# Performance work log

Measured on AMD Instinct MI355X. Metric: run time of the kernel, lower is better.

Reference implementation:

```python
import jax, jax.numpy as jnp
import numpy as np

N_NODES = 100000
HIDDEN = 64
N_REL = 9
N_LAYERS = 3
N_EDGES = 1000000


def setup_inputs() -> dict:
    key = jax.random.key(0)
    k1, k2, k3, k4, k5 = jax.random.split(key, 5)
    edge_index = jax.random.randint(k1, (2, N_EDGES), 0, N_NODES, dtype=jnp.int64)
    edge_type = jax.random.randint(k2, (N_EDGES,), 0, N_REL, dtype=jnp.int64)
    embeddings = jax.random.uniform(k3, (N_NODES, HIDDEN), dtype=jnp.float32)
    weights = jax.random.uniform(k4, (N_LAYERS, 2 * N_REL, HIDDEN, HIDDEN), dtype=jnp.float32)
    biases = jax.random.uniform(k5, (N_LAYERS, 2 * N_REL, HIDDEN), dtype=jnp.float32)
    return {"edge_index": edge_index, "edge_type": edge_type,
            "embeddings": embeddings, "weights": weights, "biases": biases}


def reference(edge_index, edge_type, embeddings, weights, biases):
    # Faithful translation of RGCNEncoder.forward.
    # NOTE (faithful to source): get_messages always reads self.embeddings,
    # and both `sources` and `dests` are edge_index[d][edge_type == r].
    N, E = embeddings.shape
    L = weights.shape[0]
    R = weights.shape[1] // 2
    idx0 = edge_index[0]          # indices for direction d=0 (source == dest)
    idx1 = edge_index[1]          # indices for direction d=1
    rel0 = edge_type              # weight row r + R*0
    rel1 = edge_type + R          # weight row r + R*1

    output = embeddings
    for l in range(L):
        # Transform every node under every (relation, direction) weight once,
        # then gather per edge. Equivalent to per-relation gather->matmul, but
        # avoids materializing per-edge [E,E] weight matrices.
        T = jnp.einsum('ne,reo->rno', embeddings, weights[l])   # [2R, N, E]
        m0 = T[rel0, idx0] + biases[l][rel0]                    # [n_edges, E]
        m1 = T[rel1, idx1] + biases[l][rel1]                    # [n_edges, E]
        m = jnp.concatenate([m0, m1], axis=0)
        d = jnp.concatenate([idx0, idx1], axis=0)
        # scatter_mean over destination nodes (0 for nodes with no messages)
        s = jax.ops.segment_sum(m, d, num_segments=N)
        cnt = jax.ops.segment_sum(jnp.ones((d.shape[0],), m.dtype), d, num_segments=N)
        hidden = jnp.where(cnt[:, None] > 0, s / jnp.maximum(cnt, 1.0)[:, None], 0.0)
        if l + 1 < L:
            hidden = jax.nn.relu(hidden)
        output = hidden
    return output
```

## Files before the change

### kernel.cpp

```cpp
#include <hip/hip_runtime.h>


typedef float  floatx4 __attribute__((ext_vector_type(4)));
typedef short  shortx8 __attribute__((ext_vector_type(8)));

#define MFMA_BF16(A, B, C) __builtin_amdgcn_mfma_f32_16x16x32_bf16((A), (B), (C), 0, 0, 0)

#define SCAT_GRID 512
#define BKT_CAP   6144

static __device__ __forceinline__ ushort f32_to_bf16_rne(float f) {
    union { float f; unsigned u; } v; v.f = f;
    unsigned r = v.u + 0x7fffu + ((v.u >> 16) & 1u);
    return (ushort)(r >> 16);
}

__global__ void rgcn_prep(const float* __restrict__ w2,
                          const float* __restrict__ b2,
                          ushort* __restrict__ wt_sw,
                          ushort* __restrict__ bias_sw) {
    int i = blockIdx.x * 256 + threadIdx.x;
    const int WELEMS = 18 * 8 * 64 * 8;
    if (i < WELEMS) {
        int r    = i >> 12;
        int rem  = i & 4095;
        int cid  = rem >> 9;
        int lane = (rem >> 3) & 63;
        int j    = i & 7;
        int nt = cid >> 1, kh = cid & 1;
        int o = nt * 16 + (lane & 15);
        int k = kh * 32 + (lane >> 4) * 8 + j;
        wt_sw[i] = f32_to_bf16_rne(w2[(r << 12) + (k << 6) + o]);
    } else {
        int i2 = i - WELEMS;
        if (i2 < 2048) {
            int nt   = i2 >> 9;
            int lane = (i2 >> 3) & 63;
            int j    = i2 & 7;
            int o  = nt * 16 + (lane & 15);
            int rr = (lane >> 4) * 8 + j;
            bias_sw[i2] = (rr < 18) ? f32_to_bf16_rne(b2[rr * 64 + o]) : (ushort)0;
        }
    }
}

__global__ void rgcn_count(const int* __restrict__ ei, const int* __restrict__ et,
                           int* __restrict__ cnts, int E, int N) {
    int e = blockIdx.x * 256 + threadIdx.x;
    if (e < E) {
        int r = et[e];
        int i0 = ei[e];
        int i1 = ei[E + e];
        if ((unsigned)r < 9u) {
            if ((unsigned)i0 < (unsigned)N) atomicAdd(&cnts[i0 * 18 + r], 1);
            if ((unsigned)i1 < (unsigned)N) atomicAdd(&cnts[i1 * 18 + 9 + r], 1);
        }
    }
}

__global__ __launch_bounds__(256) void rgcn_scatter(
    const int* __restrict__ ei,
    const int* __restrict__ et,
    unsigned*  __restrict__ cursors,
    ushort*    __restrict__ bkt,
    int E, int N)
{
    __shared__ unsigned hist[512];
    const int t = threadIdx.x;
    #pragma unroll
    for (int b = t; b < 512; b += 256) hist[b] = 0;
    __syncthreads();

    const int epb = (E + SCAT_GRID - 1) / SCAT_GRID;
    const int e0 = blockIdx.x * epb;
    const int e1 = (e0 + epb < E) ? e0 + epb : E;
    const unsigned KMAX = (unsigned)N * 18u;

    for (int e = e0 + t; e < e1; e += 256) {
        int r = et[e]; int i0 = ei[e]; int i1 = ei[E + e];
        if ((unsigned)r < 9u) {
            unsigned k0 = (unsigned)i0 * 18u + (unsigned)r;
            unsigned k1 = (unsigned)i1 * 18u + 9u + (unsigned)r;
            if (k0 < KMAX) atomicAdd(&hist[k0 >> 12], 1u);
            if (k1 < KMAX) atomicAdd(&hist[k1 >> 12], 1u);
        }
    }
    __syncthreads();

    for (int b = t; b < 512; b += 256) {
        unsigned c = hist[b];
        hist[b] = c ? atomicAdd(&cursors[b], c) : 0u;
    }
    __syncthreads();

    for (int e = e0 + t; e < e1; e += 256) {
        int r = et[e]; int i0 = ei[e]; int i1 = ei[E + e];
        if ((unsigned)r < 9u) {
            unsigned k0 = (unsigned)i0 * 18u + (unsigned)r;
            unsigned k1 = (unsigned)i1 * 18u + 9u + (unsigned)r;
            if (k0 < KMAX) {
                unsigned o = atomicAdd(&hist[k0 >> 12], 1u);
                if (o < BKT_CAP) bkt[(size_t)(k0 >> 12) * BKT_CAP + o] = (ushort)(k0 & 4095u);
            }
            if (k1 < KMAX) {
                unsigned o = atomicAdd(&hist[k1 >> 12], 1u);
                if (o < BKT_CAP) bkt[(size_t)(k1 >> 12) * BKT_CAP + o] = (ushort)(k1 & 4095u);
            }
        }
    }
}

__global__ __launch_bounds__(256) void rgcn_bucket_count(
    const ushort*   __restrict__ bkt,
    const unsigned* __restrict__ cursors,
    int*            __restrict__ cnts,
    int N)
{
    __shared__ int cnt[4096];
    const int t = threadIdx.x;
    const int b = blockIdx.x;
    #pragma unroll
    for (int i = t; i < 4096; i += 256) cnt[i] = 0;
    __syncthreads();

    unsigned n = cursors[b];
    if (n > BKT_CAP) n = BKT_CAP;
    const ushort* bp = bkt + (size_t)b * BKT_CAP;
    for (unsigned i = t; i < n; i += 256)
        atomicAdd(&cnt[bp[i]], 1);
    __syncthreads();

    const int base = b << 12;
    const int lim = N * 18;
    #pragma unroll
    for (int i = t; i < 4096; i += 256)
        if (base + i < lim) cnts[base + i] = cnt[i];
}

__global__ __launch_bounds__(256, 3) void rgcn_main(
    const float*  __restrict__ emb,
    const int*    __restrict__ cnts,
    const ushort* __restrict__ wt_sw,
    const ushort* __restrict__ bias_sw,
    float*        __restrict__ out,
    int N)
{
    __shared__ float  wft[18][128];
    __shared__ ushort wb[128][32];
    __shared__ int    craw[128 * 18];

    const int t    = threadIdx.x;
    const int nb   = blockIdx.x * 128;
    const int wave = t >> 6;
    const int lane = t & 63;
    const int m    = lane & 15;
    const int q    = lane >> 4;

    {
        int lim = (N - nb) * 18;
        if (lim > 2304) lim = 2304;
        #pragma unroll
        for (int j = t; j < 2304; j += 256)
            craw[j] = (j < lim) ? cnts[(size_t)nb * 18 + j] : 0;
    }

    shortx8 af[2][2];
    #pragma unroll
    for (int mt = 0; mt < 2; mt++) {
        int n = nb + wave * 32 + mt * 16 + m;
        if (n >= N) n = N - 1;
        const float* rp = emb + (size_t)n * 64 + q * 8;
        #pragma unroll
        for (int kh = 0; kh < 2; kh++) {
            floatx4 lo = *(const floatx4*)(rp + kh * 32);
            floatx4 hi = *(const floatx4*)(rp + kh * 32 + 4);
            shortx8 f;
            #pragma unroll
            for (int j = 0; j < 4; j++) {
                f[j]     = (short)f32_to_bf16_rne(lo[j]);
                f[j + 4] = (short)f32_to_bf16_rne(hi[j]);
            }
            af[mt][kh] = f;
        }
    }

    const ushort* wbase = wt_sw + (size_t)lane * 8;
    shortx8 bfA[8], bfB[8];
    #pragma unroll
    for (int c = 0; c < 8; c++) bfA[c] = *(const shortx8*)(wbase + c * 512);

    __syncthreads();

    if (t < 128) {
        int c[18];
        int cnt = 0;
        #pragma unroll
        for (int r = 0; r < 18; r++) { c[r] = craw[t * 18 + r]; cnt += c[r]; }
        float inv = (cnt > 0) ? (1.0f / (float)cnt) : 0.0f;
        #pragma unroll
        for (int r = 0; r < 18; r++) {
            float w = (float)c[r] * inv;
            wft[r][t] = w;
            wb[t][r] = f32_to_bf16_rne(w);
        }
        #pragma unroll
        for (int r = 18; r < 32; r++) wb[t][r] = 0;
    }

    __syncthreads();

    floatx4 acc[2][4];
    #pragma unroll
    for (int mt = 0; mt < 2; mt++)
        #pragma unroll
        for (int nt = 0; nt < 4; nt++)
            acc[mt][nt] = (floatx4){0.f, 0.f, 0.f, 0.f};

    for (int r = 0; r < 18; r += 2) {
        {
            const ushort* p = wbase + (r + 1) * 4096;
            #pragma unroll
            for (int c = 0; c < 8; c++) bfB[c] = *(const shortx8*)(p + c * 512);
        }
        {
            floatx4 swv[2];
            #pragma unroll
            for (int mt = 0; mt < 2; mt++)
                swv[mt] = *(const floatx4*)&wft[r][wave * 32 + mt * 16 + q * 4];
            #pragma unroll
            for (int nt = 0; nt < 4; nt++)
                #pragma unroll
                for (int mt = 0; mt < 2; mt++) {
                    floatx4 tmp = (floatx4){0.f, 0.f, 0.f, 0.f};
                    tmp = MFMA_BF16(af[mt][0], bfA[nt * 2 + 0], tmp);
                    tmp = MFMA_BF16(af[mt][1], bfA[nt * 2 + 1], tmp);
                    acc[mt][nt] += swv[mt] * tmp;
                }
        }
        if (r + 2 < 18) {
            const ushort* p = wbase + (r + 2) * 4096;
            #pragma unroll
            for (int c = 0; c < 8; c++) bfA[c] = *(const shortx8*)(p + c * 512);
        }
        {
            floatx4 swv[2];
            #pragma unroll
            for (int mt = 0; mt < 2; mt++)
                swv[mt] = *(const floatx4*)&wft[r + 1][wave * 32 + mt * 16 + q * 4];
            #pragma unroll
            for (int nt = 0; nt < 4; nt++)
                #pragma unroll
                for (int mt = 0; mt < 2; mt++) {
                    floatx4 tmp = (floatx4){0.f, 0.f, 0.f, 0.f};
                    tmp = MFMA_BF16(af[mt][0], bfB[nt * 2 + 0], tmp);
                    tmp = MFMA_BF16(af[mt][1], bfB[nt * 2 + 1], tmp);
                    acc[mt][nt] += swv[mt] * tmp;
                }
        }
    }

    {
        shortx8 wfrag[2];
        #pragma unroll
        for (int mt = 0; mt < 2; mt++)
            wfrag[mt] = *(const shortx8*)&wb[wave * 32 + mt * 16 + m][q * 8];
        #pragma unroll
        for (int nt = 0; nt < 4; nt++) {
            shortx8 btf = *(const shortx8*)(bias_sw + ((size_t)nt * 64 + lane) * 8);
            #pragma unroll
            for (int mt = 0; mt < 2; mt++)
                acc[mt][nt] = MFMA_BF16(wfrag[mt], btf, acc[mt][nt]);
        }
    }

    #pragma unroll
    for (int mt = 0; mt < 2; mt++)
        #pragma unroll
        for (int i = 0; i < 4; i++) {
            int nn = nb + wave * 32 + mt * 16 + q * 4 + i;
            if (nn < N) {
                #pragma unroll
                for (int nt = 0; nt < 4; nt++)
                    out[(size_t)nn * 64 + nt * 16 + m] = acc[mt][nt][i];
            }
        }
}

extern "C" void kernel_launch(void* const* d_in, const int* in_sizes, int n_in,
                              void* d_out, int out_size, void* d_ws, size_t ws_size,
                              hipStream_t stream) {
    const int*   edge_index = (const int*)d_in[0];
    const int*   edge_type  = (const int*)d_in[1];
    const float* emb        = (const float*)d_in[2];
    const float* weights    = (const float*)d_in[3];
    const float* biases     = (const float*)d_in[4];
    float* out = (float*)d_out;

    const int E = in_sizes[1];
    const int N = in_sizes[2] / 64;

    const float* w2 = weights + 2 * 18 * 64 * 64;
    const float* b2 = biases  + 2 * 18 * 64;

    size_t off = 0;
    unsigned* cursors = (unsigned*)((char*)d_ws + off);  off += 512 * 4;
    off = (off + 63) & ~size_t(63);
    int* cnts = (int*)((char*)d_ws + off);               off += (size_t)N * 18 * 4;
    off = (off + 63) & ~size_t(63);
    ushort* bkt = (ushort*)((char*)d_ws + off);          off += (size_t)512 * BKT_CAP * 2;
    off = (off + 63) & ~size_t(63);
    ushort* wt_sw = (ushort*)((char*)d_ws + off);        off += 73728 * 2;
    off = (off + 63) & ~size_t(63);
    ushort* bias_sw = (ushort*)((char*)d_ws + off);      off += 2048 * 2;
    size_t need = off;

    int nbuckets = (N * 18 + 4095) >> 12;

    {
        int total = 18 * 8 * 64 * 8 + 2048;
        rgcn_prep<<<(total + 255) / 256, 256, 0, stream>>>(w2, b2, wt_sw, bias_sw);
    }

    if (ws_size >= need && nbuckets <= 512) {
        hipMemsetAsync(cursors, 0, 512 * 4, stream);
        rgcn_scatter<<<SCAT_GRID, 256, 0, stream>>>(edge_index, edge_type, cursors, bkt, E, N);
        rgcn_bucket_count<<<nbuckets, 256, 0, stream>>>(bkt, cursors, cnts, N);
    } else {
        cnts = (int*)((char*)d_ws + 64);
        wt_sw = (ushort*)((char*)cnts + (size_t)N * 18 * 4);
        bias_sw = wt_sw + 73728;
        rgcn_prep<<<(18 * 8 * 64 * 8 + 2048 + 255) / 256, 256, 0, stream>>>(w2, b2, wt_sw, bias_sw);
        hipMemsetAsync(cnts, 0, (size_t)N * 18 * 4, stream);
        rgcn_count<<<(E + 255) / 256, 256, 0, stream>>>(edge_index, edge_type, cnts, E, N);
    }

    rgcn_main<<<(N + 127) / 128, 256, 0, stream>>>(emb, cnts, wt_sw, bias_sw, out, N);
}
```

Measured before the change: 150.9 us.

## Use per-block LDS bins for edge bucketing and stage weights in LDS

Edge bucketing changes: each scatter block bins its keys into fixed 32-slot LDS bins and writes them out contiguously. This removes the global cursor atomics, the memset and the two-pass histogram, but keys beyond a bin's capacity are silently dropped. Computing the per-node mean weights moves into a separate kernel that writes float and bf16 weight tables to global memory. The main kernel becomes persistent with 512 threads and loads the full bf16 weight set (about 147 KB) into LDS once per block, so weight reads per tile come from LDS rather than global memory. A global-memory fallback remains in case the LDS attribute cannot be set.

```diff
diff --git a/kernel.cpp b/kernel.cpp
--- a/kernel.cpp
+++ b/kernel.cpp
@@ -3,16 +3,24 @@
 
 typedef float  floatx4 __attribute__((ext_vector_type(4)));
 typedef short  shortx8 __attribute__((ext_vector_type(8)));
+typedef unsigned int uint;
 
 #define MFMA_BF16(A, B, C) __builtin_amdgcn_mfma_f32_16x16x32_bf16((A), (B), (C), 0, 0, 0)
 
-#define SCAT_GRID 512
-#define BKT_CAP   6144
+#define NBUF 512
+#define NBKT 512
+#define CAP  32
 
 static __device__ __forceinline__ ushort f32_to_bf16_rne(float f) {
     union { float f; unsigned u; } v; v.f = f;
     unsigned r = v.u + 0x7fffu + ((v.u >> 16) & 1u);
     return (ushort)(r >> 16);
+}
+
+static __device__ __forceinline__ void gload_lds16(const ushort* g, ushort* l) {
+    __builtin_amdgcn_global_load_lds(
+        (const __attribute__((address_space(1))) void*)g,
+        (__attribute__((address_space(3))) void*)l, 16, 0, 0);
 }
 
 __global__ void rgcn_prep(const float* __restrict__ w2,
@@ -44,6 +52,92 @@
     }
 }
 
+__global__ __launch_bounds__(256) void rgcn_scatter(
+    const int* __restrict__ ei,
+    const int* __restrict__ et,
+    ushort*    __restrict__ cursors_g,
+    ushort*    __restrict__ bkt,
+    int E, int N)
+{
+    __shared__ uint   cur[NBKT];
+    __shared__ ushort bins[NBKT][CAP];
+    const int t = threadIdx.x;
+    #pragma unroll
+    for (int b = t; b < NBKT; b += 256) cur[b] = 0;
+    __syncthreads();
+
+    const int epb = (E + NBUF - 1) / NBUF;
+    const int e0 = blockIdx.x * epb;
+    const int e1 = (e0 + epb < E) ? e0 + epb : E;
+    const unsigned KMAX = (unsigned)N * 18u;
+
+    for (int e = e0 + t; e < e1; e += 256) {
+        int r = et[e]; int i0 = ei[e]; int i1 = ei[E + e];
+        if ((unsigned)r < 9u) {
+            unsigned k0 = (unsigned)i0 * 18u + (unsigned)r;
+            unsigned k1 = (unsigned)i1 * 18u + 9u + (unsigned)r;
+            if (k0 < KMAX) {
+                unsigned o = atomicAdd(&cur[k0 >> 12], 1u);
+                if (o < CAP) bins[k0 >> 12][o] = (ushort)(k0 & 4095u);
+            }
+            if (k1 < KMAX) {
+                unsigned o = atomicAdd(&cur[k1 >> 12], 1u);
+                if (o < CAP) bins[k1 >> 12][o] = (ushort)(k1 & 4095u);
+            }
+        }
+    }
+    __syncthreads();
+
+    const uint* b32 = (const uint*)bins;
+    uint* dst = (uint*)bkt;
+    const int blk = blockIdx.x;
+    #pragma unroll
+    for (int idx = t; idx < NBKT * CAP / 2; idx += 256) {
+        int b = idx >> 4;
+        int w = idx & 15;
+        dst[((size_t)b * NBUF + blk) * (CAP / 2) + w] = b32[idx];
+    }
+    #pragma unroll
+    for (int b = t; b < NBKT; b += 256) {
+        uint c = cur[b];
+        cursors_g[(size_t)blk * NBKT + b] = (ushort)(c < CAP ? c : CAP);
+    }
+}
+
+__global__ __launch_bounds__(256) void rgcn_bucket_count(
+    const ushort* __restrict__ bkt,
+    const ushort* __restrict__ cursors_g,
+    int*          __restrict__ cnts,
+    int KMAX)
+{
+    __shared__ int    cnt[4096];
+    __shared__ ushort ccur[NBUF];
+    const int t = threadIdx.x;
+    const int b = blockIdx.x;
+    #pragma unroll
+    for (int i = t; i < 4096; i += 256) cnt[i] = 0;
+    #pragma unroll
+    for (int sb = t; sb < NBUF; sb += 256) ccur[sb] = cursors_g[(size_t)sb * NBKT + b];
+    __syncthreads();
+
+    const uint* src = (const uint*)(bkt + (size_t)b * NBUF * CAP);
+    #pragma unroll
+    for (int idx = t; idx < NBUF * CAP / 2; idx += 256) {
+        int sb = idx >> 4;
+        int w  = idx & 15;
+        unsigned c = ccur[sb];
+        unsigned v = src[idx];
+        if ((unsigned)(2 * w)     < c) atomicAdd(&cnt[v & 4095u], 1);
+        if ((unsigned)(2 * w + 1) < c) atomicAdd(&cnt[(v >> 16) & 4095u], 1);
+    }
+    __syncthreads();
+
+    const int base = b << 12;
+    #pragma unroll
+    for (int i = t; i < 4096; i += 256)
+        if (base + i < KMAX) cnts[base + i] = cnt[i];
+}
+
 __global__ void rgcn_count(const int* __restrict__ ei, const int* __restrict__ et,
                            int* __restrict__ cnts, int E, int N) {
     int e = blockIdx.x * 256 + threadIdx.x;
@@ -58,97 +152,182 @@
     }
 }
 
-__global__ __launch_bounds__(256) void rgcn_scatter(
-    const int* __restrict__ ei,
-    const int* __restrict__ et,
-    unsigned*  __restrict__ cursors,
-    ushort*    __restrict__ bkt,
-    int E, int N)
-{
-    __shared__ unsigned hist[512];
-    const int t = threadIdx.x;
-    #pragma unroll
-    for (int b = t; b < 512; b += 256) hist[b] = 0;
-    __syncthreads();
-
-    const int epb = (E + SCAT_GRID - 1) / SCAT_GRID;
-    const int e0 = blockIdx.x * epb;
-    const int e1 = (e0 + epb < E) ? e0 + epb : E;
-    const unsigned KMAX = (unsigned)N * 18u;
-
-    for (int e = e0 + t; e < e1; e += 256) {
-        int r = et[e]; int i0 = ei[e]; int i1 = ei[E + e];
-        if ((unsigned)r < 9u) {
-            unsigned k0 = (unsigned)i0 * 18u + (unsigned)r;
-            unsigned k1 = (unsigned)i1 * 18u + 9u + (unsigned)r;
-            if (k0 < KMAX) atomicAdd(&hist[k0 >> 12], 1u);
-            if (k1 < KMAX) atomicAdd(&hist[k1 >> 12], 1u);
-        }
-    }
-    __syncthreads();
-
-    for (int b = t; b < 512; b += 256) {
-        unsigned c = hist[b];
-        hist[b] = c ? atomicAdd(&cursors[b], c) : 0u;
-    }
-    __syncthreads();
-
-    for (int e = e0 + t; e < e1; e += 256) {
-        int r = et[e]; int i0 = ei[e]; int i1 = ei[E + e];
-        if ((unsigned)r < 9u) {
-            unsigned k0 = (unsigned)i0 * 18u + (unsigned)r;
-            unsigned k1 = (unsigned)i1 * 18u + 9u + (unsigned)r;
-            if (k0 < KMAX) {
-                unsigned o = atomicAdd(&hist[k0 >> 12], 1u);
-                if (o < BKT_CAP) bkt[(size_t)(k0 >> 12) * BKT_CAP + o] = (ushort)(k0 & 4095u);
-            }
-            if (k1 < KMAX) {
-                unsigned o = atomicAdd(&hist[k1 >> 12], 1u);
-                if (o < BKT_CAP) bkt[(size_t)(k1 >> 12) * BKT_CAP + o] = (ushort)(k1 & 4095u);
-            }
-        }
-    }
-}
-
-__global__ __launch_bounds__(256) void rgcn_bucket_count(
-    const ushort*   __restrict__ bkt,
-    const unsigned* __restrict__ cursors,
-    int*            __restrict__ cnts,
-    int N)
-{
-    __shared__ int cnt[4096];
-    const int t = threadIdx.x;
-    const int b = blockIdx.x;
-    #pragma unroll
-    for (int i = t; i < 4096; i += 256) cnt[i] = 0;
-    __syncthreads();
-
-    unsigned n = cursors[b];
-    if (n > BKT_CAP) n = BKT_CAP;
-    const ushort* bp = bkt + (size_t)b * BKT_CAP;
-    for (unsigned i = t; i < n; i += 256)
-        atomicAdd(&cnt[bp[i]], 1);
-    __syncthreads();
-
-    const int base = b << 12;
-    const int lim = N * 18;
-    #pragma unroll
-    for (int i = t; i < 4096; i += 256)
-        if (base + i < lim) cnts[base + i] = cnt[i];
-}
-
-__global__ __launch_bounds__(256, 3) void rgcn_main(
+__global__ void rgcn_weights(const int* __restrict__ cnts,
+                             float*  __restrict__ wf,
+                             ushort* __restrict__ wb,
+                             int N, int Npad)
+{
+    int n = blockIdx.x * 256 + threadIdx.x;
+    if (n >= Npad) return;
+    float w[18];
+    if (n < N) {
+        int c[18]; int cnt = 0;
+        const int* cp = cnts + (size_t)n * 18;
+        #pragma unroll
+        for (int r = 0; r < 18; r++) { c[r] = cp[r]; cnt += c[r]; }
+        float inv = (cnt > 0) ? (1.0f / (float)cnt) : 0.0f;
+        #pragma unroll
+        for (int r = 0; r < 18; r++) w[r] = (float)c[r] * inv;
+    } else {
+        #pragma unroll
+        for (int r = 0; r < 18; r++) w[r] = 0.0f;
+    }
+    #pragma unroll
+    for (int r = 0; r < 18; r++) wf[(size_t)r * Npad + n] = w[r];
+    ushort pk[32];
+    #pragma unroll
+    for (int r = 0; r < 18; r++) pk[r] = f32_to_bf16_rne(w[r]);
+    #pragma unroll
+    for (int r = 18; r < 32; r++) pk[r] = 0;
+    uint4* dst = (uint4*)(wb + (size_t)n * 32);
+    const uint4* srcp = (const uint4*)pk;
+    #pragma unroll
+    for (int i = 0; i < 4; i++) dst[i] = srcp[i];
+}
+
+static __device__ __forceinline__ void mfma_r_step(
+    const shortx8 af[2][2], const shortx8 bf[8], const floatx4 swv[2], floatx4 acc[2][4])
+{
+    #pragma unroll
+    for (int nt = 0; nt < 4; nt++)
+        #pragma unroll
+        for (int mt = 0; mt < 2; mt++) {
+            floatx4 tmp = (floatx4){0.f, 0.f, 0.f, 0.f};
+            tmp = MFMA_BF16(af[mt][0], bf[nt * 2 + 0], tmp);
+            tmp = MFMA_BF16(af[mt][1], bf[nt * 2 + 1], tmp);
+            acc[mt][nt] += swv[mt] * tmp;
+        }
+}
+
+static __device__ __forceinline__ void load_af(
+    const float* __restrict__ emb, int n, int q, shortx8 af[2])
+{
+    const float* rp = emb + (size_t)n * 64 + q * 8;
+    #pragma unroll
+    for (int kh = 0; kh < 2; kh++) {
+        floatx4 lo = *(const floatx4*)(rp + kh * 32);
+        floatx4 hi = *(const floatx4*)(rp + kh * 32 + 4);
+        shortx8 f;
+        #pragma unroll
+        for (int j = 0; j < 4; j++) {
+            f[j]     = (short)f32_to_bf16_rne(lo[j]);
+            f[j + 4] = (short)f32_to_bf16_rne(hi[j]);
+        }
+        af[kh] = f;
+    }
+}
+
+__global__ __launch_bounds__(512) void rgcn_main_lds(
     const float*  __restrict__ emb,
-    const int*    __restrict__ cnts,
+    const float*  __restrict__ wf,
+    const ushort* __restrict__ wb,
     const ushort* __restrict__ wt_sw,
     const ushort* __restrict__ bias_sw,
     float*        __restrict__ out,
-    int N)
-{
-    __shared__ float  wft[18][128];
-    __shared__ ushort wb[128][32];
-    __shared__ int    craw[128 * 18];
-
+    int N, int Npad, int ntiles)
+{
+    extern __shared__ ushort wlds[];
+
+    const int t    = threadIdx.x;
+    const int wave = t >> 6;
+    const int lane = t & 63;
+    const int m    = lane & 15;
+    const int q    = lane >> 4;
+
+    for (int c = t; c < 9216; c += 512)
+        gload_lds16(wt_sw + (size_t)c * 8, wlds + (size_t)c * 8);
+    __syncthreads();
+
+    const ushort* lbase = wlds + (size_t)lane * 8;
+
+    for (int tile = blockIdx.x; tile < ntiles; tile += gridDim.x) {
+        const int nb = tile * 256;
+
+        shortx8 af[2][2];
+        #pragma unroll
+        for (int mt = 0; mt < 2; mt++) {
+            int n = nb + wave * 32 + mt * 16 + m;
+            if (n >= N) n = N - 1;
+            load_af(emb, n, q, af[mt]);
+        }
+
+        floatx4 acc[2][4];
+        #pragma unroll
+        for (int mt = 0; mt < 2; mt++)
+            #pragma unroll
+            for (int nt = 0; nt < 4; nt++)
+                acc[mt][nt] = (floatx4){0.f, 0.f, 0.f, 0.f};
+
+        const int rowbase = nb + wave * 32;
+
+        shortx8 bA[8], bB[8];
+        #pragma unroll
+        for (int c = 0; c < 8; c++) bA[c] = *(const shortx8*)(lbase + c * 512);
+
+        for (int r = 0; r < 18; r += 2) {
+            {
+                const ushort* p = lbase + (size_t)(r + 1) * 4096;
+                #pragma unroll
+                for (int c = 0; c < 8; c++) bB[c] = *(const shortx8*)(p + c * 512);
+            }
+            {
+                floatx4 swv[2];
+                #pragma unroll
+                for (int mt = 0; mt < 2; mt++)
+                    swv[mt] = *(const floatx4*)(wf + (size_t)r * Npad + rowbase + mt * 16 + q * 4);
+                mfma_r_step(af, bA, swv, acc);
+            }
+            if (r + 2 < 18) {
+                const ushort* p = lbase + (size_t)(r + 2) * 4096;
+                #pragma unroll
+                for (int c = 0; c < 8; c++) bA[c] = *(const shortx8*)(p + c * 512);
+            }
+            {
+                floatx4 swv[2];
+                #pragma unroll
+                for (int mt = 0; mt < 2; mt++)
+                    swv[mt] = *(const floatx4*)(wf + (size_t)(r + 1) * Npad + rowbase + mt * 16 + q * 4);
+                mfma_r_step(af, bB, swv, acc);
+            }
+        }
+
+        {
+            shortx8 wfrag[2];
+            #pragma unroll
+            for (int mt = 0; mt < 2; mt++)
+                wfrag[mt] = *(const shortx8*)(wb + (size_t)(rowbase + mt * 16 + m) * 32 + q * 8);
+            #pragma unroll
+            for (int nt = 0; nt < 4; nt++) {
+                shortx8 btf = *(const shortx8*)(bias_sw + ((size_t)nt * 64 + lane) * 8);
+                #pragma unroll
+                for (int mt = 0; mt < 2; mt++)
+                    acc[mt][nt] = MFMA_BF16(wfrag[mt], btf, acc[mt][nt]);
+            }
+        }
+
+        #pragma unroll
+        for (int mt = 0; mt < 2; mt++)
+            #pragma unroll
+            for (int i = 0; i < 4; i++) {
+                int nn = rowbase + mt * 16 + q * 4 + i;
+                if (nn < N) {
+                    #pragma unroll
+                    for (int nt = 0; nt < 4; nt++)
+                        out[(size_t)nn * 64 + nt * 16 + m] = acc[mt][nt][i];
+                }
+            }
+    }
+}
+
+__global__ __launch_bounds__(256, 3) void rgcn_main_glb(
+    const float*  __restrict__ emb,
+    const float*  __restrict__ wf,
+    const ushort* __restrict__ wb,
+    const ushort* __restrict__ wt_sw,
+    const ushort* __restrict__ bias_sw,
+    float*        __restrict__ out,
+    int N, int Npad)
+{
     const int t    = threadIdx.x;
     const int nb   = blockIdx.x * 128;
     const int wave = t >> 6;
@@ -156,58 +335,19 @@
     const int m    = lane & 15;
     const int q    = lane >> 4;
 
-    {
-        int lim = (N - nb) * 18;
-        if (lim > 2304) lim = 2304;
-        #pragma unroll
-        for (int j = t; j < 2304; j += 256)
-            craw[j] = (j < lim) ? cnts[(size_t)nb * 18 + j] : 0;
-    }
-
     shortx8 af[2][2];
     #pragma unroll
     for (int mt = 0; mt < 2; mt++) {
         int n = nb + wave * 32 + mt * 16 + m;
         if (n >= N) n = N - 1;
-        const float* rp = emb + (size_t)n * 64 + q * 8;
-        #pragma unroll
-        for (int kh = 0; kh < 2; kh++) {
-            floatx4 lo = *(const floatx4*)(rp + kh * 32);
-            floatx4 hi = *(const floatx4*)(rp + kh * 32 + 4);
-            shortx8 f;
-            #pragma unroll
-            for (int j = 0; j < 4; j++) {
-                f[j]     = (short)f32_to_bf16_rne(lo[j]);
-                f[j + 4] = (short)f32_to_bf16_rne(hi[j]);
-            }
-            af[mt][kh] = f;
-        }
+        load_af(emb, n, q, af[mt]);
     }
 
     const ushort* wbase = wt_sw + (size_t)lane * 8;
-    shortx8 bfA[8], bfB[8];
-    #pragma unroll
-    for (int c = 0; c < 8; c++) bfA[c] = *(const shortx8*)(wbase + c * 512);
-
-    __syncthreads();
-
-    if (t < 128) {
-        int c[18];
-        int cnt = 0;
-        #pragma unroll
-        for (int r = 0; r < 18; r++) { c[r] = craw[t * 18 + r]; cnt += c[r]; }
-        float inv = (cnt > 0) ? (1.0f / (float)cnt) : 0.0f;
-        #pragma unroll
-        for (int r = 0; r < 18; r++) {
-            float w = (float)c[r] * inv;
-            wft[r][t] = w;
-            wb[t][r] = f32_to_bf16_rne(w);
-        }
-        #pragma unroll
-        for (int r = 18; r < 32; r++) wb[t][r] = 0;
-    }
-
-    __syncthreads();
+    const int rowbase = nb + wave * 32;
+    shortx8 bA[8], bB[8];
+    #pragma unroll
+    for (int c = 0; c < 8; c++) bA[c] = *(const shortx8*)(wbase + c * 512);
 
     floatx4 acc[2][4];
     #pragma unroll
@@ -218,44 +358,28 @@
 
     for (int r = 0; r < 18; r += 2) {
         {
-            const ushort* p = wbase + (r + 1) * 4096;
-            #pragma unroll
-            for (int c = 0; c < 8; c++) bfB[c] = *(const shortx8*)(p + c * 512);
+            const ushort* p = wbase + (size_t)(r + 1) * 4096;
+            #pragma unroll
+            for (int c = 0; c < 8; c++) bB[c] = *(const shortx8*)(p + c * 512);
         }
         {
             floatx4 swv[2];
             #pragma unroll
             for (int mt = 0; mt < 2; mt++)
-                swv[mt] = *(const floatx4*)&wft[r][wave * 32 + mt * 16 + q * 4];
-            #pragma unroll
-            for (int nt = 0; nt < 4; nt++)
-                #pragma unroll
-                for (int mt = 0; mt < 2; mt++) {
-                    floatx4 tmp = (floatx4){0.f, 0.f, 0.f, 0.f};
-                    tmp = MFMA_BF16(af[mt][0], bfA[nt * 2 + 0], tmp);
-                    tmp = MFMA_BF16(af[mt][1], bfA[nt * 2 + 1], tmp);
-                    acc[mt][nt] += swv[mt] * tmp;
-                }
+                swv[mt] = *(const floatx4*)(wf + (size_t)r * Npad + rowbase + mt * 16 + q * 4);
+            mfma_r_step(af, bA, swv, acc);
         }
         if (r + 2 < 18) {
-            const ushort* p = wbase + (r + 2) * 4096;
-            #pragma unroll
-            for (int c = 0; c < 8; c++) bfA[c] = *(const shortx8*)(p + c * 512);
+            const ushort* p = wbase + (size_t)(r + 2) * 4096;
+            #pragma unroll
+            for (int c = 0; c < 8; c++) bA[c] = *(const shortx8*)(p + c * 512);
         }
         {
             floatx4 swv[2];
             #pragma unroll
             for (int mt = 0; mt < 2; mt++)
-                swv[mt] = *(const floatx4*)&wft[r + 1][wave * 32 + mt * 16 + q * 4];
-            #pragma unroll
-            for (int nt = 0; nt < 4; nt++)
-                #pragma unroll
-                for (int mt = 0; mt < 2; mt++) {
-                    floatx4 tmp = (floatx4){0.f, 0.f, 0.f, 0.f};
-                    tmp = MFMA_BF16(af[mt][0], bfB[nt * 2 + 0], tmp);
-                    tmp = MFMA_BF16(af[mt][1], bfB[nt * 2 + 1], tmp);
-                    acc[mt][nt] += swv[mt] * tmp;
-                }
+                swv[mt] = *(const floatx4*)(wf + (size_t)(r + 1) * Npad + rowbase + mt * 16 + q * 4);
+            mfma_r_step(af, bB, swv, acc);
         }
     }
 
@@ -263,7 +387,7 @@
         shortx8 wfrag[2];
         #pragma unroll
         for (int mt = 0; mt < 2; mt++)
-            wfrag[mt] = *(const shortx8*)&wb[wave * 32 + mt * 16 + m][q * 8];
+            wfrag[mt] = *(const shortx8*)(wb + (size_t)(rowbase + mt * 16 + m) * 32 + q * 8);
         #pragma unroll
         for (int nt = 0; nt < 4; nt++) {
             shortx8 btf = *(const shortx8*)(bias_sw + ((size_t)nt * 64 + lane) * 8);
@@ -277,7 +401,7 @@
     for (int mt = 0; mt < 2; mt++)
         #pragma unroll
         for (int i = 0; i < 4; i++) {
-            int nn = nb + wave * 32 + mt * 16 + q * 4 + i;
+            int nn = rowbase + mt * 16 + q * 4 + i;
             if (nn < N) {
                 #pragma unroll
                 for (int nt = 0; nt < 4; nt++)
@@ -298,41 +422,53 @@
 
     const int E = in_sizes[1];
     const int N = in_sizes[2] / 64;
+    const int Npad = ((N + 255) / 256) * 256;
+    const int ntiles = Npad / 256;
+    const int KMAX = N * 18;
+    const int nbuckets = (KMAX + 4095) >> 12;
 
     const float* w2 = weights + 2 * 18 * 64 * 64;
     const float* b2 = biases  + 2 * 18 * 64;
 
     size_t off = 0;
-    unsigned* cursors = (unsigned*)((char*)d_ws + off);  off += 512 * 4;
-    off = (off + 63) & ~size_t(63);
-    int* cnts = (int*)((char*)d_ws + off);               off += (size_t)N * 18 * 4;
-    off = (off + 63) & ~size_t(63);
-    ushort* bkt = (ushort*)((char*)d_ws + off);          off += (size_t)512 * BKT_CAP * 2;
-    off = (off + 63) & ~size_t(63);
-    ushort* wt_sw = (ushort*)((char*)d_ws + off);        off += 73728 * 2;
-    off = (off + 63) & ~size_t(63);
-    ushort* bias_sw = (ushort*)((char*)d_ws + off);      off += 2048 * 2;
+    auto take = [&](size_t bytes) { void* p = (char*)d_ws + off; off = (off + bytes + 63) & ~(size_t)63; return p; };
+    ushort* cursors_g = (ushort*)take((size_t)NBUF * NBKT * 2);
+    ushort* bkt       = (ushort*)take((size_t)NBKT * NBUF * CAP * 2);
+    int*    cnts      = (int*)take((size_t)KMAX * 4);
+    float*  wf        = (float*)take((size_t)18 * Npad * 4);
+    ushort* wb        = (ushort*)take((size_t)Npad * 32 * 2);
+    ushort* wt_sw     = (ushort*)take(73728 * 2);
+    ushort* bias_sw   = (ushort*)take(2048 * 2);
     size_t need = off;
 
-    int nbuckets = (N * 18 + 4095) >> 12;
-
-    {
-        int total = 18 * 8 * 64 * 8 + 2048;
-        rgcn_prep<<<(total + 255) / 256, 256, 0, stream>>>(w2, b2, wt_sw, bias_sw);
-    }
-
-    if (ws_size >= need && nbuckets <= 512) {
-        hipMemsetAsync(cursors, 0, 512 * 4, stream);
-        rgcn_scatter<<<SCAT_GRID, 256, 0, stream>>>(edge_index, edge_type, cursors, bkt, E, N);
-        rgcn_bucket_count<<<nbuckets, 256, 0, stream>>>(bkt, cursors, cnts, N);
+    rgcn_prep<<<(73728 + 2048 + 255) / 256, 256, 0, stream>>>(w2, b2, wt_sw, bias_sw);
+
+    if (ws_size >= need && nbuckets <= NBKT) {
+        rgcn_scatter<<<NBUF, 256, 0, stream>>>(edge_index, edge_type, cursors_g, bkt, E, N);
+        rgcn_bucket_count<<<nbuckets, 256, 0, stream>>>(bkt, cursors_g, cnts, KMAX);
     } else {
-        cnts = (int*)((char*)d_ws + 64);
-        wt_sw = (ushort*)((char*)cnts + (size_t)N * 18 * 4);
+        cnts    = (int*)d_ws;
+        wf      = (float*)((char*)d_ws + (((size_t)KMAX * 4 + 63) & ~(size_t)63));
+        wb      = (ushort*)((char*)wf + (size_t)18 * Npad * 4);
+        wt_sw   = (ushort*)((char*)wb + (size_t)Npad * 32 * 2);
         bias_sw = wt_sw + 73728;
-        rgcn_prep<<<(18 * 8 * 64 * 8 + 2048 + 255) / 256, 256, 0, stream>>>(w2, b2, wt_sw, bias_sw);
-        hipMemsetAsync(cnts, 0, (size_t)N * 18 * 4, stream);
+        rgcn_prep<<<(73728 + 2048 + 255) / 256, 256, 0, stream>>>(w2, b2, wt_sw, bias_sw);
+        hipMemsetAsync(cnts, 0, (size_t)KMAX * 4, stream);
         rgcn_count<<<(E + 255) / 256, 256, 0, stream>>>(edge_index, edge_type, cnts, E, N);
     }
 
-    rgcn_main<<<(N + 127) / 128, 256, 0, stream>>>(emb, cnts, wt_sw, bias_sw, out, N);
-}
+    rgcn_weights<<<Npad / 256, 256, 0, stream>>>(cnts, wf, wb, N, Npad);
+
+    const int SHMEM = 73728 * 2;
+    hipError_t attr_ok = hipFuncSetAttribute(
+        reinterpret_cast<const void*>(rgcn_main_lds),
+        hipFuncAttributeMaxDynamicSharedMemorySize, SHMEM);
+    (void)hipGetLastError();
+
+    if (attr_ok == hipSuccess) {
+        int grid = ntiles < 256 ? ntiles : 256;
+        rgcn_main_lds<<<grid, 512, SHMEM, stream>>>(emb, wf, wb, wt_sw, bias_sw, out, N, Npad, ntiles);
+    } else {
+        rgcn_main_glb<<<(N + 127) / 128, 256, 0, stream>>>(emb, wf, wb, wt_sw, bias_sw, out, N, Npad);
+    }
+}
```

Result: slower. 277.2 us (+83.7%).
